# Kernel optimization log

Hardware: AMD Instinct MI355X
Metric: run time of the kernel (lower is better)

## Reference

```python
import jax, jax.numpy as jnp
import numpy as np

# dims: B graphs, E entities, R relations, N = E + R nodes, H hidden, P prop steps
B, N, E, R, H, P, RT, NH = 4, 2048, 1600, 448, 512, 2, 100, 4
DH = H // NH  # head dim = 128


def setup_inputs() -> dict:
    key = jax.random.key(0)
    ks = jax.random.split(key, 12)
    adj = jax.random.randint(ks[0], (B, N, N), 0, 2, dtype=jnp.int32)
    # self-loops so no attention row is fully masked (avoids NaN softmax rows)
    adj = jnp.maximum(adj, jnp.eye(N, dtype=jnp.int32)[None])
    rels = jax.random.randint(ks[1], (B, R), 0, RT, dtype=jnp.int32)
    vents = jax.random.normal(ks[2], (B, E, H), jnp.float32)
    renc_w = jax.random.normal(ks[3], (RT, H), jnp.float32) * 0.05  # xavier-ish
    s = 0.02
    inp = dict(adjs=adj, rels=rels, vents=vents, entlen=E, renc_w=renc_w)
    inp["Wq"] = jax.random.normal(ks[4], (P, H, H), jnp.float32) * s
    inp["Wk"] = jax.random.normal(ks[5], (P, H, H), jnp.float32) * s
    inp["Wv"] = jax.random.normal(ks[6], (P, H, H), jnp.float32) * s
    inp["Wo"] = jax.random.normal(ks[7], (P, H, H), jnp.float32) * s
    inp["W1"] = jax.random.normal(ks[8], (P, H, 4 * H), jnp.float32) * s
    inp["W2"] = jax.random.normal(ks[9], (P, 4 * H, H), jnp.float32) * s
    inp["bq"] = jnp.zeros((P, H), jnp.float32)
    inp["bk"] = jnp.zeros((P, H), jnp.float32)
    inp["bv"] = jnp.zeros((P, H), jnp.float32)
    inp["bo"] = jnp.zeros((P, H), jnp.float32)
    inp["b1"] = jnp.zeros((P, 4 * H), jnp.float32)
    inp["b2"] = jnp.zeros((P, H), jnp.float32)
    inp["ln1_g"] = jnp.ones((P, H), jnp.float32)
    inp["ln1_b"] = jnp.zeros((P, H), jnp.float32)
    inp["ln2_g"] = jnp.ones((P, H), jnp.float32)
    inp["ln2_b"] = jnp.zeros((P, H), jnp.float32)
    inp["prelu_a"] = jnp.full((P, 4 * H), 0.25, jnp.float32)  # torch PReLU default
    return inp


def _ln(x, g, b):
    mu = x.mean(-1, keepdims=True)
    var = x.var(-1, keepdims=True)
    return (x - mu) * jax.lax.rsqrt(var + jnp.float32(1e-5)) * g + b


def reference(adjs, rels, vents, entlen, renc_w, Wq, Wk, Wv, Wo, W1, W2,
              bq, bk, bv, bo, b1, b2, ln1_g, ln1_b, ln2_g, ln2_b, prelu_a):
    vrel = renc_w[rels]                              # (B,R,H) relation embeddings
    x = jnp.concatenate([vents, vrel], axis=1)       # (B,N,H) graph node features
    neg = (adjs == 0)[:, None, :, :]                 # (B,1,N,N) True = masked
    for j in range(P):  # prop steps, structurally distinct layers
        q = (x @ Wq[j] + bq[j]).reshape(B, N, NH, DH)
        k = (x @ Wk[j] + bk[j]).reshape(B, N, NH, DH)
        v = (x @ Wv[j] + bv[j]).reshape(B, N, NH, DH)
        sc = jnp.einsum('bqhd,bkhd->bhqk', q, k) / jnp.sqrt(jnp.float32(DH))
        sc = jnp.where(neg, jnp.float32(-1e9), sc)
        a = jax.nn.softmax(sc, axis=-1)
        o = jnp.einsum('bhqk,bkhd->bqhd', a, v).reshape(B, N, H)
        attn_out = o @ Wo[j] + bo[j]
        t = _ln(attn_out, ln1_g[j], ln1_b[j])        # ln_1
        hpre = t @ W1[j] + b1[j]
        hact = jnp.where(hpre >= 0, hpre, prelu_a[j] * hpre)  # PReLU
        y = hact @ W2[j] + b2[j]                     # dropout is identity in eval
        x = _ln(y + t, ln2_g[j], ln2_b[j])           # ln_2 residual
    glob = x[:, entlen]                              # (B,H) global node = vgraph[entlens[i]]
    gents = x                                        # (B,N,H) all graphs same size -> no pad
    elens = jnp.full((B,), N, jnp.int32)
    emask = jnp.arange(N)[None, :] <= elens[:, None] # (B,N) faithful `<=` comparison
    return glob, gents, emask
```

## Files before the change

### kernel.cpp

```cpp
#include <hip/hip_runtime.h>

typedef unsigned short u16;
typedef __bf16 bf16x8 __attribute__((ext_vector_type(8)));
typedef float floatx4 __attribute__((ext_vector_type(4)));


__device__ __forceinline__ float bf2f(u16 u) {
  union { unsigned int i; float f; } c; c.i = ((unsigned int)u) << 16; return c.f;
}
__device__ __forceinline__ u16 f2bf(float f) {
  union { unsigned int i; float f; } c; c.f = f;
  unsigned int i = c.i;
  return (u16)((i + 0x7FFFu + ((i >> 16) & 1u)) >> 16);
}

__device__ __forceinline__ void gload16(const u16* __restrict__ g, u16* l) {
  __builtin_amdgcn_global_load_lds(
      (const __attribute__((address_space(1))) unsigned int*)g,
      (__attribute__((address_space(3))) unsigned int*)l, 16, 0, 0);
}

template <int EPI, int FOUT, int SEG3>
__global__ __launch_bounds__(256, 3) void gemm_tn(
    const u16* __restrict__ A, const u16* __restrict__ Bt, void* __restrict__ Cv,
    const float* __restrict__ bias, const float* __restrict__ bias2,
    const float* __restrict__ bias3, const float* __restrict__ alpha,
    const float* __restrict__ res, int K, int lda, int ldb, int ldc) {
  __shared__ __align__(16) u16 As[128 * 32];
  __shared__ __align__(16) u16 Bs[128 * 32];

  const int tid = threadIdx.x;
  const int w = tid >> 6, lane = tid & 63;
  const int quad = lane >> 4, l16 = lane & 15;
  const int wm = w & 1, wn = w >> 1;

  const int slot0 = w * 128 + lane;
  const int slot1 = slot0 + 64;
  const u16* pA0 = A + (long)(blockIdx.x * 128 + (slot0 >> 2)) * lda + (slot0 & 3) * 8;
  const u16* pA1 = A + (long)(blockIdx.x * 128 + (slot1 >> 2)) * lda + (slot1 & 3) * 8;
  const u16* pB0 = Bt + (long)(blockIdx.y * 128 + (slot0 >> 2)) * ldb + (slot0 & 3) * 8;
  const u16* pB1 = Bt + (long)(blockIdx.y * 128 + (slot1 >> 2)) * ldb + (slot1 & 3) * 8;
  u16* asd0 = As + w * 1024;
  u16* asd1 = asd0 + 512;
  u16* bsd0 = Bs + w * 1024;
  u16* bsd1 = bsd0 + 512;

  const floatx4 z4 = {0.f, 0.f, 0.f, 0.f};
  floatx4 acc[4][4];
#pragma unroll
  for (int i = 0; i < 4; i++)
#pragma unroll
    for (int j = 0; j < 4; j++) acc[i][j] = z4;

  for (int k0 = 0; k0 < K; k0 += 32) {
    __syncthreads();
    gload16(pA0, asd0);
    gload16(pA1, asd1);
    gload16(pB0, bsd0);
    gload16(pB1, bsd1);
    pA0 += 32; pA1 += 32; pB0 += 32; pB1 += 32;
    __syncthreads();

    bf16x8 af[4], bv[4];
#pragma unroll
    for (int mi = 0; mi < 4; mi++)
      af[mi] = *(const bf16x8*)&As[(wm * 64 + mi * 16 + l16) * 32 + quad * 8];
#pragma unroll
    for (int ni = 0; ni < 4; ni++)
      bv[ni] = *(const bf16x8*)&Bs[(wn * 64 + ni * 16 + l16) * 32 + quad * 8];
#pragma unroll
    for (int mi = 0; mi < 4; mi++)
#pragma unroll
      for (int ni = 0; ni < 4; ni++)
        acc[mi][ni] = __builtin_amdgcn_mfma_f32_16x16x32_bf16(af[mi], bv[ni], acc[mi][ni], 0, 0, 0);
  }

  const float* bptr = bias;
  if (SEG3) {
    const int seg = blockIdx.y >> 2;
    bptr = (seg == 0) ? bias : ((seg == 1) ? bias2 : bias3);
  }
  const long crow0 = (long)blockIdx.x * 128;
  const int ncol0 = blockIdx.y * 128 + wn * 64 + l16;
#pragma unroll
  for (int mi = 0; mi < 4; mi++) {
#pragma unroll
    for (int r = 0; r < 4; r++) {
      const int m = wm * 64 + mi * 16 + quad * 4 + r;
      const long rowbase = (crow0 + m) * (long)ldc;
      const float* rrow = (EPI == 3) ? (res + rowbase) : nullptr;
#pragma unroll
      for (int ni = 0; ni < 4; ni++) {
        const int n = ncol0 + ni * 16;
        float vv = acc[mi][ni][r] + bptr[SEG3 ? (n & 511) : n];
        if (EPI == 2) { if (vv < 0.f) vv *= alpha[n]; }
        if (EPI == 3) vv += rrow[n];
        if (FOUT) ((float*)Cv)[rowbase + n] = vv;
        else ((u16*)Cv)[rowbase + n] = f2bf(vv);
      }
    }
  }
}

template <int EPI, int FOUT>
__global__ __launch_bounds__(256, 3) void gemm_tn64(
    const u16* __restrict__ A, const u16* __restrict__ Bt, void* __restrict__ Cv,
    const float* __restrict__ bias, const float* __restrict__ alpha,
    const float* __restrict__ res, int K, int lda, int ldb, int ldc) {
  __shared__ __align__(16) u16 As[128 * 32];
  __shared__ __align__(16) u16 Bs[64 * 32];

  const int tid = threadIdx.x;
  const int w = tid >> 6, lane = tid & 63;
  const int quad = lane >> 4, l16 = lane & 15;

  const int rA0 = tid >> 2, cA = (tid & 3) * 8;
  const int rA1 = rA0 + 64;
  const u16* pA0 = A + (long)(blockIdx.x * 128 + rA0) * lda + cA;
  const u16* pA1 = A + (long)(blockIdx.x * 128 + rA1) * lda + cA;
  const u16* pB  = Bt + (long)(blockIdx.y * 64 + rA0) * ldb + cA;
  u16* asd0 = As + w * 512;
  u16* asd1 = asd0 + 2048;
  u16* bsd  = Bs + w * 512;

  const floatx4 z4 = {0.f, 0.f, 0.f, 0.f};
  floatx4 acc[2][4];
#pragma unroll
  for (int i = 0; i < 2; i++)
#pragma unroll
    for (int j = 0; j < 4; j++) acc[i][j] = z4;

  for (int k0 = 0; k0 < K; k0 += 32) {
    __syncthreads();
    gload16(pA0, asd0);
    gload16(pA1, asd1);
    gload16(pB, bsd);
    pA0 += 32; pA1 += 32; pB += 32;
    __syncthreads();

    bf16x8 af[2], bv[4];
#pragma unroll
    for (int mi = 0; mi < 2; mi++)
      af[mi] = *(const bf16x8*)&As[(w * 32 + mi * 16 + l16) * 32 + quad * 8];
#pragma unroll
    for (int ni = 0; ni < 4; ni++)
      bv[ni] = *(const bf16x8*)&Bs[(ni * 16 + l16) * 32 + quad * 8];
#pragma unroll
    for (int mi = 0; mi < 2; mi++)
#pragma unroll
      for (int ni = 0; ni < 4; ni++)
        acc[mi][ni] = __builtin_amdgcn_mfma_f32_16x16x32_bf16(af[mi], bv[ni], acc[mi][ni], 0, 0, 0);
  }

  const long crow0 = (long)blockIdx.x * 128;
  const int ncol0 = blockIdx.y * 64 + l16;
#pragma unroll
  for (int mi = 0; mi < 2; mi++) {
#pragma unroll
    for (int r = 0; r < 4; r++) {
      const int m = w * 32 + mi * 16 + quad * 4 + r;
      const long rowbase = (crow0 + m) * (long)ldc;
      const float* rrow = (EPI == 3) ? (res + rowbase) : nullptr;
#pragma unroll
      for (int ni = 0; ni < 4; ni++) {
        const int n = ncol0 + ni * 16;
        float vv = acc[mi][ni][r] + bias[n];
        if (EPI == 2) { if (vv < 0.f) vv *= alpha[n]; }
        if (EPI == 3) vv += rrow[n];
        if (FOUT) ((float*)Cv)[rowbase + n] = vv;
        else ((u16*)Cv)[rowbase + n] = f2bf(vv);
      }
    }
  }
}

#define LDP 136
__global__ __launch_bounds__(256, 3) void k_attn(
    const u16* __restrict__ qkv, const u16* __restrict__ vt,
    const unsigned* __restrict__ mbits, u16* __restrict__ og) {
  __shared__ __align__(16) u16 KV[128 * LDP];
  __shared__ __align__(16) u16 Pl[64 * LDP];
  __shared__ unsigned Ml[64 * 4];

  const int tid = threadIdx.x;
  const int w = tid >> 6, lane = tid & 63;
  const int quad = lane >> 4, l16 = lane & 15;
  const int qt = blockIdx.x;
  const int z = blockIdx.y;
  const int b = z >> 2, h = z & 3;

  const u16* qbase = qkv + (long)b * 2048 * 1536 + h * 128;
  const u16* kbase = qbase + 512;
  const u16* vbase = vt + (long)(b * 4 + h) * 128 * 2048;
  const unsigned* mbase = mbits + ((long)b * 2048 + qt * 64) * 64;

  bf16x8 qf[4];
#pragma unroll
  for (int ks = 0; ks < 4; ks++)
    qf[ks] = *(const bf16x8*)(qbase +
        (long)(qt * 64 + w * 16 + l16) * 1536 + ks * 32 + quad * 8);

  const floatx4 z4 = {0.f, 0.f, 0.f, 0.f};
  floatx4 Oacc[8];
#pragma unroll
  for (int ni = 0; ni < 8; ni++) Oacc[ni] = z4;
  float mrow[4], lrow[4];
#pragma unroll
  for (int r = 0; r < 4; r++) { mrow[r] = -3.4e38f; lrow[r] = 0.f; }

  const float scale = 0.08838834764831845f;
  const int srow = tid >> 4;
  const int scol = (tid & 15) * 8;

  for (int kt = 0; kt < 16; kt++) {
    __syncthreads();
#pragma unroll
    for (int rr = 0; rr < 128; rr += 16)
      *(int4*)&KV[(rr + srow) * LDP + scol] =
          *(const int4*)(kbase + (long)(kt * 128 + rr + srow) * 1536 + scol);
    Ml[tid] = mbase[(tid >> 2) * 64 + kt * 4 + (tid & 3)];
    __syncthreads();

    floatx4 accS[8];
#pragma unroll
    for (int ni = 0; ni < 8; ni++) accS[ni] = z4;
#pragma unroll
    for (int ks = 0; ks < 4; ks++) {
      bf16x8 bf[8];
#pragma unroll
      for (int ni = 0; ni < 8; ni++)
        bf[ni] = *(const bf16x8*)&KV[(ni * 16 + l16) * LDP + ks * 32 + quad * 8];
#pragma unroll
      for (int ni = 0; ni < 8; ni++)
        accS[ni] = __builtin_amdgcn_mfma_f32_16x16x32_bf16(qf[ks], bf[ni], accS[ni], 0, 0, 0);
    }
    __syncthreads();

#pragma unroll
    for (int rr = 0; rr < 128; rr += 16)
      *(int4*)&KV[(rr + srow) * LDP + scol] =
          *(const int4*)(vbase + (long)(rr + srow) * 2048 + kt * 128 + scol);

#pragma unroll
    for (int r = 0; r < 4; r++) {
      const int rowl = w * 16 + quad * 4 + r;
      float s[8];
      float rmax = -1e30f;
#pragma unroll
      for (int ni = 0; ni < 8; ni++) {
        const unsigned mw = Ml[rowl * 4 + (ni >> 1)];
        const int on = (mw >> ((ni & 1) * 16 + l16)) & 1;
        s[ni] = on ? accS[ni][r] * scale : -1e30f;
        rmax = fmaxf(rmax, s[ni]);
      }
#pragma unroll
      for (int off = 1; off < 16; off <<= 1) rmax = fmaxf(rmax, __shfl_xor(rmax, off, 64));
      const float mnew = fmaxf(mrow[r], rmax);
      const float al = __expf(mrow[r] - mnew);
      float rs = 0.f;
#pragma unroll
      for (int ni = 0; ni < 8; ni++) {
        const float pp = __expf(s[ni] - mnew);
        rs += pp;
        Pl[rowl * LDP + ni * 16 + l16] = f2bf(pp);
      }
#pragma unroll
      for (int off = 1; off < 16; off <<= 1) rs += __shfl_xor(rs, off, 64);
      lrow[r] = lrow[r] * al + rs;
      mrow[r] = mnew;
#pragma unroll
      for (int ni = 0; ni < 8; ni++) Oacc[ni][r] *= al;
    }
    __syncthreads();

#pragma unroll
    for (int ks = 0; ks < 4; ks++) {
      bf16x8 bv[8];
#pragma unroll
      for (int ni = 0; ni < 8; ni++)
        bv[ni] = *(const bf16x8*)&KV[(ni * 16 + l16) * LDP + ks * 32 + quad * 8];
      bf16x8 pf = *(const bf16x8*)&Pl[(w * 16 + l16) * LDP + ks * 32 + quad * 8];
#pragma unroll
      for (int ni = 0; ni < 8; ni++)
        Oacc[ni] = __builtin_amdgcn_mfma_f32_16x16x32_bf16(pf, bv[ni], Oacc[ni], 0, 0, 0);
    }
  }

#pragma unroll
  for (int r = 0; r < 4; r++) {
    const float inv = 1.f / lrow[r];
    const long q = qt * 64 + w * 16 + quad * 4 + r;
#pragma unroll
    for (int ni = 0; ni < 8; ni++)
      og[((long)b * 2048 + q) * 512 + h * 128 + ni * 16 + l16] = f2bf(Oacc[ni][r] * inv);
  }
}

__global__ __launch_bounds__(256) void k_maskpack(const int* __restrict__ adjs,
                                                  unsigned* __restrict__ bits) {
  const int wid = blockIdx.x * 4 + (threadIdx.x >> 6);
  const int lane = threadIdx.x & 63;
  const unsigned long long bal = __ballot(adjs[(long)wid * 64 + lane] != 0);
  if (lane == 0) {
    bits[wid * 2] = (unsigned)bal;
    bits[wid * 2 + 1] = (unsigned)(bal >> 32);
  }
}

__global__ __launch_bounds__(256) void tr_w(const float* __restrict__ src, u16* __restrict__ dst,
                                            int ld_src, int ld_dst, long s_z, long d_z) {
  __shared__ u16 tile[32][33];
  src += (long)blockIdx.z * s_z;
  dst += (long)blockIdx.z * d_z;
  const int r0 = blockIdx.x << 5, c0 = blockIdx.y << 5;
  const int tx = threadIdx.x & 31, ty = threadIdx.x >> 5;
#pragma unroll
  for (int i = 0; i < 32; i += 8)
    tile[ty + i][tx] = f2bf(src[(long)(r0 + ty + i) * ld_src + c0 + tx]);
  __syncthreads();
#pragma unroll
  for (int i = 0; i < 32; i += 8)
    dst[(long)(c0 + ty + i) * ld_dst + r0 + tx] = tile[tx][ty + i];
}

__global__ __launch_bounds__(256) void tr_bf16(const u16* __restrict__ src, u16* __restrict__ dst,
                                               int ld_src, int ld_dst, int zdiv,
                                               long s_out, long s_in, long d_out, long d_in_) {
  __shared__ u16 tile[32][33];
  const int zz = blockIdx.z, zq = zz / zdiv, zr = zz % zdiv;
  src += (long)zq * s_out + (long)zr * s_in;
  dst += (long)zq * d_out + (long)zr * d_in_;
  const int r0 = blockIdx.x << 5, c0 = blockIdx.y << 5;
  const int tx = threadIdx.x & 31, ty = threadIdx.x >> 5;
#pragma unroll
  for (int i = 0; i < 32; i += 8) tile[ty + i][tx] = src[(long)(r0 + ty + i) * ld_src + c0 + tx];
  __syncthreads();
#pragma unroll
  for (int i = 0; i < 32; i += 8) dst[(long)(c0 + ty + i) * ld_dst + r0 + tx] = tile[tx][ty + i];
}

__global__ __launch_bounds__(256) void k_build_x(const float* __restrict__ vents,
                                                 const int* __restrict__ rels,
                                                 const float* __restrict__ renc,
                                                 float* __restrict__ x, u16* __restrict__ xb) {
  const long idx = (long)blockIdx.x * 256 + threadIdx.x;
  const int c = (int)(idx & 511);
  const int row = (int)(idx >> 9);
  const int b = row >> 11, n = row & 2047;
  float val;
  if (n < 1600) val = vents[((long)b * 1600 + n) * 512 + c];
  else val = renc[(long)rels[b * 448 + (n - 1600)] * 512 + c];
  x[idx] = val;
  xb[idx] = f2bf(val);
}

__global__ __launch_bounds__(256) void k_ln(const float* __restrict__ in, float* __restrict__ out,
                                            u16* __restrict__ outb,
                                            const float* __restrict__ g, const float* __restrict__ bb) {
  __shared__ float rs[256], rq[256];
  const int row = blockIdx.x, tid = threadIdx.x;
  const float* p = in + (long)row * 512;
  const float a0 = p[tid], a1 = p[tid + 256];
  rs[tid] = a0 + a1;
  rq[tid] = a0 * a0 + a1 * a1;
  __syncthreads();
  for (int s = 128; s > 0; s >>= 1) {
    if (tid < s) { rs[tid] += rs[tid + s]; rq[tid] += rq[tid + s]; }
    __syncthreads();
  }
  const float mu = rs[0] * (1.f / 512.f);
  const float var = rq[0] * (1.f / 512.f) - mu * mu;
  const float inv = 1.0f / sqrtf(var + 1e-5f);
  const float o0 = (a0 - mu) * inv * g[tid] + bb[tid];
  const float o1 = (a1 - mu) * inv * g[tid + 256] + bb[tid + 256];
  out[(long)row * 512 + tid] = o0;
  out[(long)row * 512 + tid + 256] = o1;
  outb[(long)row * 512 + tid] = f2bf(o0);
  outb[(long)row * 512 + tid + 256] = f2bf(o1);
}

__global__ __launch_bounds__(256) void k_out(const float* __restrict__ x, const int* __restrict__ entlen,
                                             float* __restrict__ out, long out_n) {
  const long idx = (long)blockIdx.x * 256 + threadIdx.x;
  if (idx >= out_n) return;
  const long G = 2048, GE = 2048 + 4194304;
  float v;
  if (idx < G) {
    const int b = (int)(idx >> 9), c = (int)(idx & 511);
    int e = entlen[0];
    if (e < 0 || e >= 2048) e = 1600;
    v = x[((long)b * 2048 + e) * 512 + c];
  } else if (idx < GE) {
    v = x[idx - G];
  } else {
    v = 1.0f;
  }
  out[idx] = v;
}

extern "C" void kernel_launch(void* const* d_in, const int* in_sizes, int n_in,
                              void* d_out, int out_size, void* d_ws, size_t ws_size,
                              hipStream_t stream) {
  const int* adjs = (const int*)d_in[0];
  const int* rels = (const int*)d_in[1];
  const float* vents = (const float*)d_in[2];
  const int* entlen = (const int*)d_in[3];
  const float* renc = (const float*)d_in[4];
  const float* Wq = (const float*)d_in[5];
  const float* Wk = (const float*)d_in[6];
  const float* Wv = (const float*)d_in[7];
  const float* Wo = (const float*)d_in[8];
  const float* W1 = (const float*)d_in[9];
  const float* W2 = (const float*)d_in[10];
  const float* bq = (const float*)d_in[11];
  const float* bk = (const float*)d_in[12];
  const float* bv = (const float*)d_in[13];
  const float* bo = (const float*)d_in[14];
  const float* b1 = (const float*)d_in[15];
  const float* b2 = (const float*)d_in[16];
  const float* ln1g = (const float*)d_in[17];
  const float* ln1b = (const float*)d_in[18];
  const float* ln2g = (const float*)d_in[19];
  const float* ln2b = (const float*)d_in[20];
  const float* prelu = (const float*)d_in[21];

  char* base = (char*)d_ws;
  float* x_f   = (float*)(base + 0);
  float* t_f   = (float*)(base + 16777216);
  float* tmp_f = (float*)(base + 33554432);
  u16* wt  = (u16*)(base + 50331648);
  u16* xb  = (u16*)(base + 62914560);
  u16* tb  = (u16*)(base + 71303168);
  u16* qkv = (u16*)(base + 79691776);
  u16* Vtb = (u16*)(base + 104857600);
  u16* ob  = (u16*)(base + 113246208);
  u16* hb  = (u16*)(base + 121634816);
  unsigned* mbits = (unsigned*)(base + 155189248);

  k_build_x<<<dim3(16384), 256, 0, stream>>>(vents, rels, renc, x_f, xb);
  k_maskpack<<<dim3(65536), 256, 0, stream>>>(adjs, mbits);

  tr_w<<<dim3(16, 16, 2), 256, 0, stream>>>(Wq, wt + 0,       512, 512, 262144L, 3145728L);
  tr_w<<<dim3(16, 16, 2), 256, 0, stream>>>(Wk, wt + 262144,  512, 512, 262144L, 3145728L);
  tr_w<<<dim3(16, 16, 2), 256, 0, stream>>>(Wv, wt + 524288,  512, 512, 262144L, 3145728L);
  tr_w<<<dim3(16, 16, 2), 256, 0, stream>>>(Wo, wt + 786432,  512, 512, 262144L, 3145728L);
  tr_w<<<dim3(16, 64, 2), 256, 0, stream>>>(W1, wt + 1048576, 2048, 512, 1048576L, 3145728L);
  tr_w<<<dim3(64, 16, 2), 256, 0, stream>>>(W2, wt + 2097152, 512, 2048, 1048576L, 3145728L);

  for (int j = 0; j < 2; j++) {
    const u16* wqt = wt + (long)j * 3145728;
    const u16* wot = wqt + 786432;
    const u16* w1t = wqt + 1048576;
    const u16* w2t = wqt + 2097152;

    gemm_tn<1, 0, 1><<<dim3(64, 12), 256, 0, stream>>>(
        xb, wqt, qkv, bq + j * 512, bk + j * 512, bv + j * 512, nullptr, nullptr,
        512, 512, 512, 1536);

    tr_bf16<<<dim3(64, 4, 16), 256, 0, stream>>>(qkv + 1024, Vtb, 1536, 2048, 4,
        3145728L, 128L, 1048576L, 262144L);

    k_attn<<<dim3(32, 16), 256, 0, stream>>>(qkv, Vtb, mbits, ob);

    gemm_tn64<1, 1><<<dim3(64, 8), 256, 0, stream>>>(ob, wot, tmp_f, bo + j * 512, nullptr, nullptr, 512, 512, 512, 512);
    k_ln<<<dim3(8192), 256, 0, stream>>>(tmp_f, t_f, tb, ln1g + j * 512, ln1b + j * 512);
    gemm_tn<2, 0, 0><<<dim3(64, 16), 256, 0, stream>>>(tb, w1t, hb, b1 + j * 2048, nullptr, nullptr, prelu + j * 2048, nullptr, 512, 512, 512, 2048);
    gemm_tn64<3, 1><<<dim3(64, 8), 256, 0, stream>>>(hb, w2t, tmp_f, b2 + j * 512, nullptr, t_f, 2048, 2048, 2048, 512);
    k_ln<<<dim3(8192), 256, 0, stream>>>(tmp_f, x_f, xb, ln2g + j * 512, ln2b + j * 512);
  }

  const long out_n = (long)out_size;
  k_out<<<dim3((unsigned)((out_n + 255) / 256)), 256, 0, stream>>>(x_f, entlen, (float*)d_out, out_n);
}
```

Before: 632.1 us.

## Split attention over key halves with separate softmax merge kernel

The attention kernel now splits the key dimension into two halves along a new grid z dimension, so twice as many blocks are launched. Each block writes unnormalized fp32 partial outputs plus its running max and sum. A new merge kernel combines the two halves with log-sum-exp rescaling and writes the bf16 output. This aims to fill more CUs than the original 512-block grid, at the cost of extra fp32 partial traffic, an extra launch, and reuse of the x_f/t_f buffers as scratch, which must be large enough for the offsets used.

```diff
diff --git a/kernel.cpp b/kernel.cpp
--- a/kernel.cpp
+++ b/kernel.cpp
@@ -177,7 +177,8 @@
 #define LDP 136
 __global__ __launch_bounds__(256, 3) void k_attn(
     const u16* __restrict__ qkv, const u16* __restrict__ vt,
-    const unsigned* __restrict__ mbits, u16* __restrict__ og) {
+    const unsigned* __restrict__ mbits, float* __restrict__ Ob,
+    float* __restrict__ mlb) {
   __shared__ __align__(16) u16 KV[128 * LDP];
   __shared__ __align__(16) u16 Pl[64 * LDP];
   __shared__ unsigned Ml[64 * 4];
@@ -187,6 +188,7 @@
   const int quad = lane >> 4, l16 = lane & 15;
   const int qt = blockIdx.x;
   const int z = blockIdx.y;
+  const int half = blockIdx.z;
   const int b = z >> 2, h = z & 3;
 
   const u16* qbase = qkv + (long)b * 2048 * 1536 + h * 128;
@@ -212,7 +214,7 @@
   const int srow = tid >> 4;
   const int scol = (tid & 15) * 8;
 
-  for (int kt = 0; kt < 16; kt++) {
+  for (int kt = half * 8; kt < half * 8 + 8; kt++) {
     __syncthreads();
 #pragma unroll
     for (int rr = 0; rr < 128; rr += 16)
@@ -286,14 +288,34 @@
     }
   }
 
+  float* Op = Ob + (long)half * 8388608;
+  float* mlp = mlb + (long)half * 65536 + ((long)(b * 4 + h) * 2048) * 2;
 #pragma unroll
   for (int r = 0; r < 4; r++) {
-    const float inv = 1.f / lrow[r];
     const long q = qt * 64 + w * 16 + quad * 4 + r;
 #pragma unroll
     for (int ni = 0; ni < 8; ni++)
-      og[((long)b * 2048 + q) * 512 + h * 128 + ni * 16 + l16] = f2bf(Oacc[ni][r] * inv);
-  }
+      Op[((long)b * 2048 + q) * 512 + h * 128 + ni * 16 + l16] = Oacc[ni][r];
+    if (l16 == 0) { mlp[q * 2] = mrow[r]; mlp[q * 2 + 1] = lrow[r]; }
+  }
+}
+
+__global__ __launch_bounds__(256) void k_attnmerge(
+    const float* __restrict__ Ob, const float* __restrict__ mlb,
+    u16* __restrict__ og) {
+  const long idx = (long)blockIdx.x * 256 + threadIdx.x;
+  const int c = (int)(idx & 511);
+  const long row = idx >> 9;
+  const int b = (int)(row >> 11), q = (int)(row & 2047);
+  const int h = c >> 7;
+  const long mlo = ((long)(b * 4 + h) * 2048 + q) * 2;
+  const float m0 = mlb[mlo], l0 = mlb[mlo + 1];
+  const float m1 = mlb[65536 + mlo], l1 = mlb[65536 + mlo + 1];
+  const float M = fmaxf(m0, m1);
+  const float e0 = __expf(m0 - M), e1 = __expf(m1 - M);
+  const float L = l0 * e0 + l1 * e1;
+  const float o = (Ob[idx] * e0 + Ob[8388608 + idx] * e1) / L;
+  og[idx] = f2bf(o);
 }
 
 __global__ __launch_bounds__(256) void k_maskpack(const int* __restrict__ adjs,
@@ -460,7 +482,8 @@
     tr_bf16<<<dim3(64, 4, 16), 256, 0, stream>>>(qkv + 1024, Vtb, 1536, 2048, 4,
         3145728L, 128L, 1048576L, 262144L);
 
-    k_attn<<<dim3(32, 16), 256, 0, stream>>>(qkv, Vtb, mbits, ob);
+    k_attn<<<dim3(32, 16, 2), 256, 0, stream>>>(qkv, Vtb, mbits, x_f, t_f);
+    k_attnmerge<<<dim3(16384), 256, 0, stream>>>(x_f, t_f, ob);
 
     gemm_tn64<1, 1><<<dim3(64, 8), 256, 0, stream>>>(ob, wot, tmp_f, bo + j * 512, nullptr, nullptr, 512, 512, 512, 512);
     k_ln<<<dim3(8192), 256, 0, stream>>>(tmp_f, t_f, tb, ln1g + j * 512, ln1b + j * 512);
```

After: 647.5 us. 1.02x slower.

## Double-buffer LDS tiles in GEMM kernels to overlap loads with MFMA

Applied to the files above, without the earlier changes.

Both GEMM kernels now use two LDS buffers per operand. The next K-slice is issued via global_load_lds into the alternate buffer before the MFMAs run on the current one, with a single barrier per iteration instead of two. The aim is to hide global-load latency behind compute and cut barrier stalls. In exchange, LDS use per block doubles, which may lower occupancy. Correctness relies on the barrier waiting for outstanding async LDS loads (vmcnt) before the next iteration reads that buffer.

```diff
diff --git a/kernel.cpp b/kernel.cpp
--- a/kernel.cpp
+++ b/kernel.cpp
@@ -26,8 +26,8 @@
     const float* __restrict__ bias, const float* __restrict__ bias2,
     const float* __restrict__ bias3, const float* __restrict__ alpha,
     const float* __restrict__ res, int K, int lda, int ldb, int ldc) {
-  __shared__ __align__(16) u16 As[128 * 32];
-  __shared__ __align__(16) u16 Bs[128 * 32];
+  __shared__ __align__(16) u16 As[2][128 * 32];
+  __shared__ __align__(16) u16 Bs[2][128 * 32];
 
   const int tid = threadIdx.x;
   const int w = tid >> 6, lane = tid & 63;
@@ -40,10 +40,8 @@
   const u16* pA1 = A + (long)(blockIdx.x * 128 + (slot1 >> 2)) * lda + (slot1 & 3) * 8;
   const u16* pB0 = Bt + (long)(blockIdx.y * 128 + (slot0 >> 2)) * ldb + (slot0 & 3) * 8;
   const u16* pB1 = Bt + (long)(blockIdx.y * 128 + (slot1 >> 2)) * ldb + (slot1 & 3) * 8;
-  u16* asd0 = As + w * 1024;
-  u16* asd1 = asd0 + 512;
-  u16* bsd0 = Bs + w * 1024;
-  u16* bsd1 = bsd0 + 512;
+  const int woff0 = w * 1024;
+  const int woff1 = woff0 + 512;
 
   const floatx4 z4 = {0.f, 0.f, 0.f, 0.f};
   floatx4 acc[4][4];
@@ -52,27 +50,38 @@
 #pragma unroll
     for (int j = 0; j < 4; j++) acc[i][j] = z4;
 
+  gload16(pA0, &As[0][woff0]);
+  gload16(pA1, &As[0][woff1]);
+  gload16(pB0, &Bs[0][woff0]);
+  gload16(pB1, &Bs[0][woff1]);
+  pA0 += 32; pA1 += 32; pB0 += 32; pB1 += 32;
+  __syncthreads();
+
+  int p = 0;
   for (int k0 = 0; k0 < K; k0 += 32) {
-    __syncthreads();
-    gload16(pA0, asd0);
-    gload16(pA1, asd1);
-    gload16(pB0, bsd0);
-    gload16(pB1, bsd1);
-    pA0 += 32; pA1 += 32; pB0 += 32; pB1 += 32;
-    __syncthreads();
+    if (k0 + 32 < K) {
+      gload16(pA0, &As[p ^ 1][woff0]);
+      gload16(pA1, &As[p ^ 1][woff1]);
+      gload16(pB0, &Bs[p ^ 1][woff0]);
+      gload16(pB1, &Bs[p ^ 1][woff1]);
+      pA0 += 32; pA1 += 32; pB0 += 32; pB1 += 32;
+    }
 
     bf16x8 af[4], bv[4];
 #pragma unroll
     for (int mi = 0; mi < 4; mi++)
-      af[mi] = *(const bf16x8*)&As[(wm * 64 + mi * 16 + l16) * 32 + quad * 8];
+      af[mi] = *(const bf16x8*)&As[p][(wm * 64 + mi * 16 + l16) * 32 + quad * 8];
 #pragma unroll
     for (int ni = 0; ni < 4; ni++)
-      bv[ni] = *(const bf16x8*)&Bs[(wn * 64 + ni * 16 + l16) * 32 + quad * 8];
+      bv[ni] = *(const bf16x8*)&Bs[p][(wn * 64 + ni * 16 + l16) * 32 + quad * 8];
 #pragma unroll
     for (int mi = 0; mi < 4; mi++)
 #pragma unroll
       for (int ni = 0; ni < 4; ni++)
         acc[mi][ni] = __builtin_amdgcn_mfma_f32_16x16x32_bf16(af[mi], bv[ni], acc[mi][ni], 0, 0, 0);
+
+    __syncthreads();
+    p ^= 1;
   }
 
   const float* bptr = bias;
@@ -107,8 +116,8 @@
     const u16* __restrict__ A, const u16* __restrict__ Bt, void* __restrict__ Cv,
     const float* __restrict__ bias, const float* __restrict__ alpha,
     const float* __restrict__ res, int K, int lda, int ldb, int ldc) {
-  __shared__ __align__(16) u16 As[128 * 32];
-  __shared__ __align__(16) u16 Bs[64 * 32];
+  __shared__ __align__(16) u16 As[2][128 * 32];
+  __shared__ __align__(16) u16 Bs[2][64 * 32];
 
   const int tid = threadIdx.x;
   const int w = tid >> 6, lane = tid & 63;
@@ -119,9 +128,9 @@
   const u16* pA0 = A + (long)(blockIdx.x * 128 + rA0) * lda + cA;
   const u16* pA1 = A + (long)(blockIdx.x * 128 + rA1) * lda + cA;
   const u16* pB  = Bt + (long)(blockIdx.y * 64 + rA0) * ldb + cA;
-  u16* asd0 = As + w * 512;
-  u16* asd1 = asd0 + 2048;
-  u16* bsd  = Bs + w * 512;
+  const int aoff0 = w * 512;
+  const int aoff1 = aoff0 + 2048;
+  const int boff  = w * 512;
 
   const floatx4 z4 = {0.f, 0.f, 0.f, 0.f};
   floatx4 acc[2][4];
@@ -130,26 +139,36 @@
 #pragma unroll
     for (int j = 0; j < 4; j++) acc[i][j] = z4;
 
+  gload16(pA0, &As[0][aoff0]);
+  gload16(pA1, &As[0][aoff1]);
+  gload16(pB, &Bs[0][boff]);
+  pA0 += 32; pA1 += 32; pB += 32;
+  __syncthreads();
+
+  int p = 0;
   for (int k0 = 0; k0 < K; k0 += 32) {
-    __syncthreads();
-    gload16(pA0, asd0);
-    gload16(pA1, asd1);
-    gload16(pB, bsd);
-    pA0 += 32; pA1 += 32; pB += 32;
-    __syncthreads();
+    if (k0 + 32 < K) {
+      gload16(pA0, &As[p ^ 1][aoff0]);
+      gload16(pA1, &As[p ^ 1][aoff1]);
+      gload16(pB, &Bs[p ^ 1][boff]);
+      pA0 += 32; pA1 += 32; pB += 32;
+    }
 
     bf16x8 af[2], bv[4];
 #pragma unroll
     for (int mi = 0; mi < 2; mi++)
-      af[mi] = *(const bf16x8*)&As[(w * 32 + mi * 16 + l16) * 32 + quad * 8];
+      af[mi] = *(const bf16x8*)&As[p][(w * 32 + mi * 16 + l16) * 32 + quad * 8];
 #pragma unroll
     for (int ni = 0; ni < 4; ni++)
-      bv[ni] = *(const bf16x8*)&Bs[(ni * 16 + l16) * 32 + quad * 8];
+      bv[ni] = *(const bf16x8*)&Bs[p][(ni * 16 + l16) * 32 + quad * 8];
 #pragma unroll
     for (int mi = 0; mi < 2; mi++)
 #pragma unroll
       for (int ni = 0; ni < 4; ni++)
         acc[mi][ni] = __builtin_amdgcn_mfma_f32_16x16x32_bf16(af[mi], bv[ni], acc[mi][ni], 0, 0, 0);
+
+    __syncthreads();
+    p ^= 1;
   }
 
   const long crow0 = (long)blockIdx.x * 128;
```

Result: no change. 629.7 us (-0.4%).
